# Performance work log

Measured on AMD Instinct MI355X. Metric: run time of the kernel, lower is better.

The kernel has to match this reference:

```python
import jax, jax.numpy as jnp
import numpy as np

B, S, E, H, D, P = 4, 2048, 1024, 16, 64, 64  # batch, seq, embed, heads, head_dim, position_dim
MASKED_BIAS = -10000.0


def setup_inputs() -> dict:
    key = jax.random.key(0)
    ks = jax.random.split(key, 24)
    n = lambda k, sh: jax.random.normal(k, sh, dtype=jnp.float32)
    eyeD = jnp.eye(D, dtype=jnp.float32)
    eyeH = jnp.eye(H, dtype=jnp.float32)
    inp = {
        'hidden_states': n(ks[0], (B, S, E)),
        'position_states': n(ks[1], (B, S, P)),
        # Conv2D per-head projections (identity init + perturbation): [H, D, D]
        'Wq': eyeD[None] + 0.02 * n(ks[2], (H, D, D)), 'bq': 0.01 * n(ks[3], (H, D)),
        'Wk': eyeD[None] + 0.02 * n(ks[4], (H, D, D)), 'bk': 0.01 * n(ks[5], (H, D)),
        'Wv': eyeD[None] + 0.02 * n(ks[6], (H, D, D)), 'bv': 0.01 * n(ks[7], (H, D)),
        # Conv2D(transpose=True) cross-head mix: weight [H_out, H_in, D], bias [H, D]
        'Wqh': eyeH[:, :, None] + 0.02 * n(ks[8], (H, H, D)), 'bqh': 0.01 * n(ks[9], (H, D)),
        'Wkh': eyeH[:, :, None] + 0.02 * n(ks[10], (H, H, D)), 'bkh': 0.01 * n(ks[11], (H, D)),
        'Wvh': eyeH[:, :, None] + 0.02 * n(ks[12], (H, H, D)), 'bvh': 0.01 * n(ks[13], (H, D)),
        # p_attn Conv1D: position_dim -> 3*head_dim
        'Wp': 0.02 * n(ks[14], (P, 3 * D)), 'bp': 0.01 * n(ks[15], (3 * D,)),
        # position_conv expand: weight [3, 1, H], bias [H]
        'Wpe': 0.02 * n(ks[16], (3, 1, H)), 'bpe': 0.01 * n(ks[17], (H,)),
        # c_proj Conv1D: E -> E
        'Wc': 0.02 * n(ks[18], (E, E)), 'bc': 0.01 * n(ks[19], (E,)),
    }
    return inp


def _attention(hidden_states, position_states, Wq, bq, Wqh, bqh, Wk, bk, Wkh, bkh,
               Wv, bv, Wvh, bvh, Wp, bp, Wpe, bpe, Wc, bc):
    b, s, _ = hidden_states.shape
    x = hidden_states.reshape(b, s, H, D)

    def proj(Wa, ba, Wh, bh):
        # Conv2D: per-head linear within head_dim
        y = jnp.einsum('bshd,hde->bshe', x, Wa) + ba
        # Conv2D(transpose): mix across heads, per feature dim d
        return jnp.einsum('bshd,ghd->bsgd', y, Wh) + bh

    q = proj(Wq, bq, Wqh, bqh)  # [b,s,H,D]
    k = proj(Wk, bk, Wkh, bkh)
    v = proj(Wv, bv, Wvh, bvh)

    # p_attn (Conv1D) -> [b,s,3,D]; p_expand broadcasts each var across heads
    p = (position_states @ Wp + bp).reshape(b, s, 3, D)
    pe = p[..., None, :] * Wpe[:, 0, :][:, :, None] + bpe[:, None]  # [b,s,3,H,D]
    q = q + pe[:, :, 0]
    k = k + pe[:, :, 1]
    v = v + pe[:, :, 2]

    q = q.transpose(0, 2, 1, 3)  # [b,H,s,D]
    k = k.transpose(0, 2, 1, 3)
    v = v.transpose(0, 2, 1, 3)

    scores = jnp.einsum('bhqd,bhkd->bhqk', q, k) / jnp.sqrt(jnp.float32(D))
    causal = jnp.tril(jnp.ones((s, s), dtype=bool))
    scores = jnp.where(causal, scores, jnp.float32(MASKED_BIAS))
    w = jax.nn.softmax(scores, axis=-1)
    o = jnp.einsum('bhqk,bhkd->bhqd', w, v)
    o = o.transpose(0, 2, 1, 3).reshape(b, s, E)
    return o @ Wc + bc


def reference(hidden_states, position_states, Wq, bq, Wqh, bqh, Wk, bk, Wkh, bkh,
              Wv, bv, Wvh, bvh, Wp, bp, Wpe, bpe, Wc, bc):
    return _attention(hidden_states, position_states, Wq, bq, Wqh, bqh, Wk, bk,
                      Wkh, bkh, Wv, bv, Wvh, bvh, Wp, bp, Wpe, bpe, Wc, bc)
```

## Files before the change

### kernel.cpp

```cpp
#include <hip/hip_runtime.h>
#include <stdint.h>
#include <stddef.h>

using bf16x8 = __attribute__((ext_vector_type(8))) __bf16;
using f32x4  = __attribute__((ext_vector_type(4))) float;
using u16x8  = __attribute__((ext_vector_type(8))) unsigned short;
using u16x4  = __attribute__((ext_vector_type(4))) unsigned short;
typedef unsigned short u16;

#define DEV __device__ __forceinline__

#define QSCALE 0.18033688011112042f
#define SBIAS 32.0f

DEV u16 f2bf(float f) {
  unsigned u = __float_as_uint(f);
  u += 0x7fffu + ((u >> 16) & 1u);
  return (u16)(u >> 16);
}

DEV void gld_lds16(const u16* g, u16* l) {
  __builtin_amdgcn_global_load_lds(
      (__attribute__((address_space(1))) void*)g,
      (__attribute__((address_space(3))) void*)l, 16, 0, 0);
}

__global__ __launch_bounds__(256) void k_prep(const float* __restrict__ hs, const float* __restrict__ ps,
                                              const float* __restrict__ Wq, const float* __restrict__ Wk,
                                              const float* __restrict__ Wv, const float* __restrict__ Wqh,
                                              const float* __restrict__ Wkh, const float* __restrict__ Wvh,
                                              const float* __restrict__ Wp, const float* __restrict__ Wpe,
                                              const float* __restrict__ bq, const float* __restrict__ bk,
                                              const float* __restrict__ bv, const float* __restrict__ bqh,
                                              const float* __restrict__ bkh, const float* __restrict__ bvh,
                                              const float* __restrict__ bp, const float* __restrict__ bpe,
                                              const float* __restrict__ Wc,
                                              u16* __restrict__ A, u16* __restrict__ Wt,
                                              float* __restrict__ bias, u16* __restrict__ WcT) {
  const int bid = blockIdx.x;
  if (bid < 8704) {
    int idx = bid * 256 + threadIdx.x;
    int t  = idx / 272;
    int c4 = (idx - t * 272) * 4;
    float4 f;
    if (c4 < 1024) f = *(const float4*)(hs + (size_t)t * 1024 + c4);
    else           f = *(const float4*)(ps + (size_t)t * 64 + (c4 - 1024));
    u16x4 o4;
    o4[0] = f2bf(f.x); o4[1] = f2bf(f.y); o4[2] = f2bf(f.z); o4[3] = f2bf(f.w);
    *(u16x4*)(A + (size_t)t * 1088 + c4) = o4;
  } else if (bid < 21760) {
    int idx = (bid - 8704) * 256 + threadIdx.x;
    int n = idx / 1088, kk = idx - n * 1088;
    int which = n >> 10, g = (n >> 6) & 15, e = n & 63;
    const float* Wa = (which == 0) ? Wq : (which == 1) ? Wk : Wv;
    const float* Wh = (which == 0) ? Wqh : (which == 1) ? Wkh : Wvh;
    float val;
    if (kk < 1024) {
      int h = kk >> 6, d = kk & 63;
      val = Wa[(size_t)(h * 64 + d) * 64 + e] * Wh[(size_t)(g * 16 + h) * 64 + e];
    } else {
      int p = kk - 1024;
      val = Wp[(size_t)p * 192 + which * 64 + e] * Wpe[which * 16 + g];
    }
    if (which == 0) val *= QSCALE;
    Wt[idx] = f2bf(val);
  } else if (bid < 21772) {
    int n = (bid - 21760) * 256 + threadIdx.x;
    int which = n >> 10, g = (n >> 6) & 15, e = n & 63;
    const float* ba = (which == 0) ? bq : (which == 1) ? bk : bv;
    const float* Wh = (which == 0) ? Wqh : (which == 1) ? Wkh : Wvh;
    const float* bh = (which == 0) ? bqh : (which == 1) ? bkh : bvh;
    float s = bh[g * 64 + e] + bp[which * 64 + e] * Wpe[which * 16 + g] + bpe[g];
    for (int h = 0; h < 16; ++h) s += ba[h * 64 + e] * Wh[(g * 16 + h) * 64 + e];
    if (which == 0) s *= QSCALE;
    bias[n] = s;
  } else {
    __shared__ float tile[32][33];
    int t = bid - 21772;
    int tx = threadIdx.x & 31, ty = threadIdx.x >> 5;
    int n0 = (t & 31) * 32, k0 = (t >> 5) * 32;
#pragma unroll
    for (int i = 0; i < 32; i += 8)
      tile[ty + i][tx] = Wc[(size_t)(k0 + ty + i) * 1024 + n0 + tx];
    __syncthreads();
#pragma unroll
    for (int i = 0; i < 32; i += 8)
      WcT[(size_t)(n0 + ty + i) * 1024 + k0 + tx] = f2bf(tile[tx][ty + i]);
  }
}

template <int EPI>
__global__ __launch_bounds__(256) void gemm128(const u16* __restrict__ A, const u16* __restrict__ Bt,
                                               const float* __restrict__ bias,
                                               u16* __restrict__ qo, u16* __restrict__ ko, u16* __restrict__ vo,
                                               float* __restrict__ outf, int M, int N, int K, int NT) {
  __shared__ alignas(16) u16 As[2][8192];
  __shared__ alignas(16) u16 Bs[2][8192];
  const int tid = threadIdx.x;
  const int l = tid & 63, w = tid >> 6;
  const int lr = l & 15, lg = l >> 4;
  const int wm = w >> 1, wn = w & 1;

  const int nwg = gridDim.x;
  const int cpx = nwg >> 3;
  const int virt = (blockIdx.x & 7) * cpx + (blockIdx.x >> 3);
  const int m0 = (virt / NT) * 128, n0 = (virt - (virt / NT) * NT) * 128;

  const int KT = K >> 6;

  f32x4 acc[4][4] = {};

#pragma unroll
  for (int call = 0; call < 4; ++call) {
    int ci = (call * 4 + w) * 64 + l;
    int row = ci >> 3, s = ci & 7;
    int kq = (s ^ (row & 7)) * 8;
    gld_lds16(A + (size_t)(m0 + row) * K + kq, &As[0][(call * 4 + w) * 512]);
    gld_lds16(Bt + (size_t)(n0 + row) * K + kq, &Bs[0][(call * 4 + w) * 512]);
  }

  int cur = 0;
  for (int kt = 0; kt < KT; ++kt) {
    if (kt + 1 < KT) {
      const int kb = (kt + 1) * 64;
#pragma unroll
      for (int call = 0; call < 4; ++call) {
        int ci = (call * 4 + w) * 64 + l;
        int row = ci >> 3, s = ci & 7;
        int kq = (s ^ (row & 7)) * 8;
        gld_lds16(A + (size_t)(m0 + row) * K + kb + kq, &As[cur ^ 1][(call * 4 + w) * 512]);
        gld_lds16(Bt + (size_t)(n0 + row) * K + kb + kq, &Bs[cur ^ 1][(call * 4 + w) * 512]);
      }
      asm volatile("s_waitcnt vmcnt(8)" ::: "memory");
    } else {
      asm volatile("s_waitcnt vmcnt(0)" ::: "memory");
    }
    __builtin_amdgcn_s_barrier();
    asm volatile("" ::: "memory");

    const u16* AsC = As[cur];
    const u16* BsC = Bs[cur];
#pragma unroll
    for (int kk = 0; kk < 2; ++kk) {
      bf16x8 af[4], bfr[4];
#pragma unroll
      for (int mf = 0; mf < 4; ++mf) {
        int row = wm * 64 + mf * 16 + lr;
        int byo = row * 128 + (((kk * 32 + lg * 8) * 2) ^ ((row & 7) << 4));
        af[mf] = *(const bf16x8*)((const char*)AsC + byo);
      }
#pragma unroll
      for (int nf = 0; nf < 4; ++nf) {
        int row = wn * 64 + nf * 16 + lr;
        int byo = row * 128 + (((kk * 32 + lg * 8) * 2) ^ ((row & 7) << 4));
        bfr[nf] = *(const bf16x8*)((const char*)BsC + byo);
      }
      __builtin_amdgcn_s_setprio(1);
#pragma unroll
      for (int mf = 0; mf < 4; ++mf)
#pragma unroll
        for (int nf = 0; nf < 4; ++nf)
          acc[mf][nf] = __builtin_amdgcn_mfma_f32_16x16x32_bf16(af[mf], bfr[nf], acc[mf][nf], 0, 0, 0);
      __builtin_amdgcn_s_setprio(0);
    }

    asm volatile("s_waitcnt lgkmcnt(0)" ::: "memory");
    __builtin_amdgcn_s_barrier();
    asm volatile("" ::: "memory");
    cur ^= 1;
  }

#pragma unroll
  for (int mf = 0; mf < 4; ++mf)
#pragma unroll
    for (int nf = 0; nf < 4; ++nf)
#pragma unroll
      for (int r = 0; r < 4; ++r) {
        int row = m0 + wm * 64 + mf * 16 + lg * 4 + r;
        int col = n0 + wn * 64 + nf * 16 + lr;
        float val = acc[mf][nf][r] + bias[col];
        if (EPI == 0) {
          int which = col >> 10, g = (col >> 6) & 15, e = col & 63;
          int b = row >> 11, si = row & 2047;
          size_t idx = ((size_t)((b * 16 + g) * 2048 + si)) * 64 + e;
          u16 bvv = f2bf(val);
          if (which == 0) qo[idx] = bvv;
          else if (which == 1) ko[idx] = bvv;
          else vo[idx] = bvv;
        } else {
          outf[(size_t)row * N + col] = val;
        }
      }
}

__global__ __launch_bounds__(256) void k_transV(const u16* __restrict__ v, u16* __restrict__ vT) {
  __shared__ u16 t[64][65];
  int bh = blockIdx.y, s0 = blockIdx.x * 64;
  const u16* src = v + ((size_t)bh * 2048 + s0) * 64;
  u16* dst = vT + (size_t)bh * 64 * 2048 + s0;
  int tid = threadIdx.x;
#pragma unroll
  for (int it = 0; it < 2; ++it) {
    int ci = it * 256 + tid;
    int row = ci >> 3, sl = ci & 7;
    u16x8 val = *(const u16x8*)(src + (size_t)row * 64 + sl * 8);
#pragma unroll
    for (int jj = 0; jj < 8; ++jj) t[row][sl * 8 + jj] = val[jj];
  }
  __syncthreads();
#pragma unroll
  for (int it = 0; it < 2; ++it) {
    int ci = it * 256 + tid;
    int d = ci >> 3, sl = ci & 7;
    u16x8 val;
#pragma unroll
    for (int jj = 0; jj < 8; ++jj) {
      int cp = sl * 8 + jj;
      int tt = (cp & 3) * 16 + (cp >> 2);
      val[jj] = t[tt][d];
    }
    *(u16x8*)(dst + (size_t)d * 2048 + sl * 8) = val;
  }
}

__global__ __launch_bounds__(512) void k_attn(const u16* __restrict__ q, const u16* __restrict__ k,
                                              const u16* __restrict__ vt, u16* __restrict__ o) {
  __shared__ alignas(16) u16 Ks[2][4096];
  __shared__ alignas(16) u16 Vs[2][4096];
  __shared__ alignas(16) u16 Ps[8][32 * 72];

  const int tid = threadIdx.x, l = tid & 63, w = tid >> 6;
  const int lr = l & 15, lg = l >> 4;
  const int i = blockIdx.x;
  const int bh = (i & 7) * 8 + ((i >> 3) & 7);
  const int xb = i >> 6;
  const int b = bh >> 4, h = bh & 15;

  const u16* qp = q + (size_t)bh * 2048 * 64;
  const u16* kp = k + (size_t)bh * 2048 * 64;
  const u16* vp = vt + (size_t)bh * 64 * 2048;

  const int srow = tid >> 3;
  const int skq = ((tid & 7) ^ (srow & 7)) * 8;

  bf16x8 ones;
#pragma unroll
  for (int e = 0; e < 8; ++e) ones[e] = (__bf16)1.0f;

  for (int half = 0; half < 2; ++half) {
    const int tile = half ? (7 - xb) : xb;
    const int qr0 = tile * 256 + w * 32;
    const int jmax = 4 * tile + 3;
    const int jmask = qr0 >> 6;

    bf16x8 qf[2][2];
#pragma unroll
    for (int mf = 0; mf < 2; ++mf)
#pragma unroll
      for (int kk = 0; kk < 2; ++kk)
        qf[mf][kk] = *(const bf16x8*)(qp + (size_t)(qr0 + mf * 16 + lr) * 64 + kk * 32 + lg * 8);

    f32x4 oacc[2][4] = {};
    f32x4 osum[2] = {};

    gld_lds16(kp + (size_t)srow * 64 + skq, &Ks[0][w * 512]);
    gld_lds16(vp + (size_t)srow * 2048 + skq, &Vs[0][w * 512]);

    int cur = 0;
    for (int j = 0; j <= jmax; ++j) {
      if (j < jmax) {
        const int jn = j + 1;
        gld_lds16(kp + (size_t)(jn * 64 + srow) * 64 + skq, &Ks[cur ^ 1][w * 512]);
        gld_lds16(vp + (size_t)srow * 2048 + jn * 64 + skq, &Vs[cur ^ 1][w * 512]);
        asm volatile("s_waitcnt vmcnt(2)" ::: "memory");
      } else {
        asm volatile("s_waitcnt vmcnt(0)" ::: "memory");
      }
      __builtin_amdgcn_s_barrier();
      asm volatile("" ::: "memory");

      if (j <= jmask) {
        const u16* KsC = Ks[cur];
        const u16* VsC = Vs[cur];

        f32x4 sfr[2][4];
#pragma unroll
        for (int mf = 0; mf < 2; ++mf)
#pragma unroll
          for (int nf = 0; nf < 4; ++nf)
            sfr[mf][nf] = f32x4{-SBIAS, -SBIAS, -SBIAS, -SBIAS};
#pragma unroll
        for (int kk = 0; kk < 2; ++kk) {
          bf16x8 bk[4];
#pragma unroll
          for (int nf = 0; nf < 4; ++nf) {
            int row = nf * 16 + lr;
            int byo = row * 128 + (((kk * 32 + lg * 8) * 2) ^ ((row & 7) << 4));
            bk[nf] = *(const bf16x8*)((const char*)KsC + byo);
          }
          __builtin_amdgcn_s_setprio(1);
#pragma unroll
          for (int mf = 0; mf < 2; ++mf)
#pragma unroll
            for (int nf = 0; nf < 4; ++nf)
              sfr[mf][nf] = __builtin_amdgcn_mfma_f32_16x16x32_bf16(qf[mf][kk], bk[nf], sfr[mf][nf], 0, 0, 0);
          __builtin_amdgcn_s_setprio(0);
        }

        const bool maskt = (j == jmask);
#pragma unroll
        for (int mf = 0; mf < 2; ++mf)
#pragma unroll
          for (int r = 0; r < 4; ++r) {
            float s0 = sfr[mf][0][r], s1 = sfr[mf][1][r], s2 = sfr[mf][2][r], s3 = sfr[mf][3][r];
            if (maskt) {
              int rowg = qr0 + mf * 16 + lg * 4 + r;
              int base = j * 64 + lr;
              if (base      > rowg) s0 = -1e30f;
              if (base + 16 > rowg) s1 = -1e30f;
              if (base + 32 > rowg) s2 = -1e30f;
              if (base + 48 > rowg) s3 = -1e30f;
            }
            float p0 = __builtin_amdgcn_exp2f(s0);
            float p1 = __builtin_amdgcn_exp2f(s1);
            float p2 = __builtin_amdgcn_exp2f(s2);
            float p3 = __builtin_amdgcn_exp2f(s3);
            unsigned w0, w1;
            asm("v_cvt_pk_bf16_f32 %0, %1, %2" : "=v"(w0) : "v"(p0), "v"(p1));
            asm("v_cvt_pk_bf16_f32 %0, %1, %2" : "=v"(w1) : "v"(p2), "v"(p3));
            uint2 pw; pw.x = w0; pw.y = w1;
            *(uint2*)&Ps[w][(mf * 16 + lg * 4 + r) * 72 + 4 * lr] = pw;
          }

#pragma unroll
        for (int kk = 0; kk < 2; ++kk) {
          bf16x8 pa[2];
#pragma unroll
          for (int mf = 0; mf < 2; ++mf)
            pa[mf] = *(const bf16x8*)&Ps[w][(mf * 16 + lr) * 72 + kk * 32 + lg * 8];
          bf16x8 bv[4];
#pragma unroll
          for (int df = 0; df < 4; ++df) {
            int row = df * 16 + lr;
            int byo = row * 128 + (((kk * 32 + lg * 8) * 2) ^ ((row & 7) << 4));
            bv[df] = *(const bf16x8*)((const char*)VsC + byo);
          }
          __builtin_amdgcn_s_setprio(1);
#pragma unroll
          for (int mf = 0; mf < 2; ++mf)
#pragma unroll
            for (int df = 0; df < 4; ++df)
              oacc[mf][df] = __builtin_amdgcn_mfma_f32_16x16x32_bf16(pa[mf], bv[df], oacc[mf][df], 0, 0, 0);
#pragma unroll
          for (int mf = 0; mf < 2; ++mf)
            osum[mf] = __builtin_amdgcn_mfma_f32_16x16x32_bf16(pa[mf], ones, osum[mf], 0, 0, 0);
          __builtin_amdgcn_s_setprio(0);
        }
      }

      asm volatile("s_waitcnt lgkmcnt(0)" ::: "memory");
      __builtin_amdgcn_s_barrier();
      asm volatile("" ::: "memory");
      cur ^= 1;
    }

#pragma unroll
    for (int mf = 0; mf < 2; ++mf)
#pragma unroll
      for (int r = 0; r < 4; ++r) {
        float inv = 1.0f / osum[mf][r];
        int rowg = qr0 + mf * 16 + lg * 4 + r;
#pragma unroll
        for (int df = 0; df < 4; ++df)
          o[((size_t)(b * 2048 + rowg)) * 1024 + h * 64 + df * 16 + lr] = f2bf(oacc[mf][df][r] * inv);
      }
  }
}

extern "C" void kernel_launch(void* const* d_in, const int* in_sizes, int n_in,
                              void* d_out, int out_size, void* d_ws, size_t ws_size,
                              hipStream_t stream) {
  const float* hs  = (const float*)d_in[0];
  const float* pos = (const float*)d_in[1];
  const float* Wq  = (const float*)d_in[2];  const float* bq  = (const float*)d_in[3];
  const float* Wk  = (const float*)d_in[4];  const float* bk  = (const float*)d_in[5];
  const float* Wv  = (const float*)d_in[6];  const float* bv  = (const float*)d_in[7];
  const float* Wqh = (const float*)d_in[8];  const float* bqh = (const float*)d_in[9];
  const float* Wkh = (const float*)d_in[10]; const float* bkh = (const float*)d_in[11];
  const float* Wvh = (const float*)d_in[12]; const float* bvh = (const float*)d_in[13];
  const float* Wp  = (const float*)d_in[14]; const float* bp  = (const float*)d_in[15];
  const float* Wpe = (const float*)d_in[16]; const float* bpe = (const float*)d_in[17];
  const float* Wc  = (const float*)d_in[18]; const float* bc  = (const float*)d_in[19];
  float* out = (float*)d_out;
  char* ws = (char*)d_ws;

  u16*   Abf   = (u16*)  (ws + 0);
  u16*   WT    = (u16*)  (ws + 17825792);
  float* biasq = (float*)(ws + 24510464);
  u16*   WcT   = (u16*)  (ws + 24522752);
  u16*   qb_   = (u16*)  (ws + 26619904);
  u16*   kb_   = (u16*)  (ws + 43397120);
  u16*   vb_   = (u16*)  (ws + 60174336);
  u16*   vTb   = (u16*)  (ws + 76951552);
  u16*   ob    = Abf;

  k_prep<<<22796, 256, 0, stream>>>(hs, pos, Wq, Wk, Wv, Wqh, Wkh, Wvh, Wp, Wpe,
                                    bq, bk, bv, bqh, bkh, bvh, bp, bpe, Wc,
                                    Abf, WT, biasq, WcT);
  gemm128<0><<<1536, 256, 0, stream>>>(Abf, WT, biasq, qb_, kb_, vb_, nullptr, 8192, 3072, 1088, 24);
  k_transV<<<dim3(32, 64), 256, 0, stream>>>(vb_, vTb);
  k_attn<<<256, 512, 0, stream>>>(qb_, kb_, vTb, ob);
  gemm128<1><<<512, 256, 0, stream>>>(ob, WcT, bc, nullptr, nullptr, nullptr, out, 8192, 1024, 1024, 8);
}
```

Before: 182.7 us.

## Add dedicated 256x192-tile QKV GEMM with B fragments loaded directly into registers

Replaces the templated 128x128 GEMM for the fused QKV projection with a new 512-thread kernel using 256x192 output tiles. Only A is staged through double-buffered swizzled LDS, while each wave streams its B fragments straight from global memory into registers with a one-step prefetch. The grid drops from 1536 to 512 workgroups. The aim is higher arithmetic intensity per workgroup and less LDS traffic and synchronisation. In exchange the kernel uses more registers per thread (8x3 accumulators plus 12 B vectors) and relies on hand-tuned vmcnt waits. The output-projection GEMM is de-templated to keep only the float epilogue.

```diff
diff --git a/kernel.cpp b/kernel.cpp
--- a/kernel.cpp
+++ b/kernel.cpp
@@ -89,10 +89,117 @@
   }
 }
 
-template <int EPI>
+__global__ __launch_bounds__(512) void gemmQKV(const u16* __restrict__ A, const u16* __restrict__ Bt,
+                                               const float* __restrict__ bias,
+                                               u16* __restrict__ qo, u16* __restrict__ ko, u16* __restrict__ vo,
+                                               int M, int N, int K, int NT) {
+  __shared__ alignas(16) u16 As[2][16384];
+  const int tid = threadIdx.x;
+  const int l = tid & 63, w = tid >> 6;
+  const int lr = l & 15, lg = l >> 4;
+  const int wm = w >> 2, wn = w & 3;
+
+  const int cpx = gridDim.x >> 3;
+  const int virt = (blockIdx.x & 7) * cpx + (blockIdx.x >> 3);
+  const int m0 = (virt / NT) * 256, n0 = (virt - (virt / NT) * NT) * 192;
+
+  const int KT = K >> 6;
+  const u16* bbase = Bt + (size_t)(n0 + wn * 48 + lr) * K + lg * 8;
+
+  f32x4 acc[8][3] = {};
+  bf16x8 bc0, bc1, bc2, bc3, bc4, bc5;
+  bf16x8 bn0, bn1, bn2, bn3, bn4, bn5;
+
+  bn0 = *(const bf16x8*)(bbase + (size_t)0 * K);
+  bn1 = *(const bf16x8*)(bbase + (size_t)0 * K + 32);
+  bn2 = *(const bf16x8*)(bbase + (size_t)16 * K);
+  bn3 = *(const bf16x8*)(bbase + (size_t)16 * K + 32);
+  bn4 = *(const bf16x8*)(bbase + (size_t)32 * K);
+  bn5 = *(const bf16x8*)(bbase + (size_t)32 * K + 32);
+#pragma unroll
+  for (int c = 0; c < 4; ++c) {
+    int ci = c * 512 + tid;
+    int row = ci >> 3, s = ci & 7;
+    int kq = (s ^ (row & 7)) * 8;
+    gld_lds16(A + (size_t)(m0 + row) * K + kq, &As[0][(c * 8 + w) * 512]);
+  }
+
+  for (int t = 0; t < KT; ++t) {
+    const int buf = t & 1;
+    asm volatile("s_waitcnt vmcnt(4)" ::: "memory");
+    bc0 = bn0; bc1 = bn1; bc2 = bn2; bc3 = bn3; bc4 = bn4; bc5 = bn5;
+    if (t + 1 < KT) {
+      const int kb = (t + 1) * 64;
+      bn0 = *(const bf16x8*)(bbase + (size_t)0 * K + kb);
+      bn1 = *(const bf16x8*)(bbase + (size_t)0 * K + kb + 32);
+      bn2 = *(const bf16x8*)(bbase + (size_t)16 * K + kb);
+      bn3 = *(const bf16x8*)(bbase + (size_t)16 * K + kb + 32);
+      bn4 = *(const bf16x8*)(bbase + (size_t)32 * K + kb);
+      bn5 = *(const bf16x8*)(bbase + (size_t)32 * K + kb + 32);
+#pragma unroll
+      for (int c = 0; c < 4; ++c) {
+        int ci = c * 512 + tid;
+        int row = ci >> 3, s = ci & 7;
+        int kq = (s ^ (row & 7)) * 8;
+        gld_lds16(A + (size_t)(m0 + row) * K + kb + kq, &As[buf ^ 1][(c * 8 + w) * 512]);
+      }
+      asm volatile("s_waitcnt vmcnt(10)" ::: "memory");
+    } else {
+      asm volatile("s_waitcnt vmcnt(0)" ::: "memory");
+    }
+    __builtin_amdgcn_s_barrier();
+    asm volatile("" ::: "memory");
+
+    const char* AsC = (const char*)As[buf];
+#pragma unroll
+    for (int kk = 0; kk < 2; ++kk) {
+      bf16x8 af[4];
+#pragma unroll
+      for (int half = 0; half < 2; ++half) {
+#pragma unroll
+        for (int mq = 0; mq < 4; ++mq) {
+          int row = wm * 128 + (half * 4 + mq) * 16 + lr;
+          int byo = row * 128 + (((kk * 32 + lg * 8) * 2) ^ ((row & 7) << 4));
+          af[mq] = *(const bf16x8*)(AsC + byo);
+        }
+        __builtin_amdgcn_s_setprio(1);
+#pragma unroll
+        for (int mq = 0; mq < 4; ++mq) {
+          int mf = half * 4 + mq;
+          acc[mf][0] = __builtin_amdgcn_mfma_f32_16x16x32_bf16(af[mq], kk ? bc1 : bc0, acc[mf][0], 0, 0, 0);
+          acc[mf][1] = __builtin_amdgcn_mfma_f32_16x16x32_bf16(af[mq], kk ? bc3 : bc2, acc[mf][1], 0, 0, 0);
+          acc[mf][2] = __builtin_amdgcn_mfma_f32_16x16x32_bf16(af[mq], kk ? bc5 : bc4, acc[mf][2], 0, 0, 0);
+        }
+        __builtin_amdgcn_s_setprio(0);
+      }
+    }
+
+    asm volatile("s_waitcnt lgkmcnt(0)" ::: "memory");
+    __builtin_amdgcn_s_barrier();
+    asm volatile("" ::: "memory");
+  }
+
+#pragma unroll
+  for (int mf = 0; mf < 8; ++mf)
+#pragma unroll
+    for (int nf = 0; nf < 3; ++nf)
+#pragma unroll
+      for (int r = 0; r < 4; ++r) {
+        int row = m0 + wm * 128 + mf * 16 + lg * 4 + r;
+        int col = n0 + wn * 48 + nf * 16 + lr;
+        float val = acc[mf][nf][r] + bias[col];
+        int which = col >> 10, g = (col >> 6) & 15, e = col & 63;
+        int b = row >> 11, si = row & 2047;
+        size_t idx = ((size_t)((b * 16 + g) * 2048 + si)) * 64 + e;
+        u16 bvv = f2bf(val);
+        if (which == 0) qo[idx] = bvv;
+        else if (which == 1) ko[idx] = bvv;
+        else vo[idx] = bvv;
+      }
+}
+
 __global__ __launch_bounds__(256) void gemm128(const u16* __restrict__ A, const u16* __restrict__ Bt,
                                                const float* __restrict__ bias,
-                                               u16* __restrict__ qo, u16* __restrict__ ko, u16* __restrict__ vo,
                                                float* __restrict__ outf, int M, int N, int K, int NT) {
   __shared__ alignas(16) u16 As[2][8192];
   __shared__ alignas(16) u16 Bs[2][8192];
@@ -178,18 +285,7 @@
       for (int r = 0; r < 4; ++r) {
         int row = m0 + wm * 64 + mf * 16 + lg * 4 + r;
         int col = n0 + wn * 64 + nf * 16 + lr;
-        float val = acc[mf][nf][r] + bias[col];
-        if (EPI == 0) {
-          int which = col >> 10, g = (col >> 6) & 15, e = col & 63;
-          int b = row >> 11, si = row & 2047;
-          size_t idx = ((size_t)((b * 16 + g) * 2048 + si)) * 64 + e;
-          u16 bvv = f2bf(val);
-          if (which == 0) qo[idx] = bvv;
-          else if (which == 1) ko[idx] = bvv;
-          else vo[idx] = bvv;
-        } else {
-          outf[(size_t)row * N + col] = val;
-        }
+        outf[(size_t)row * N + col] = acc[mf][nf][r] + bias[col];
       }
 }
 
@@ -407,8 +503,8 @@
   k_prep<<<22796, 256, 0, stream>>>(hs, pos, Wq, Wk, Wv, Wqh, Wkh, Wvh, Wp, Wpe,
                                     bq, bk, bv, bqh, bkh, bvh, bp, bpe, Wc,
                                     Abf, WT, biasq, WcT);
-  gemm128<0><<<1536, 256, 0, stream>>>(Abf, WT, biasq, qb_, kb_, vb_, nullptr, 8192, 3072, 1088, 24);
+  gemmQKV<<<512, 512, 0, stream>>>(Abf, WT, biasq, qb_, kb_, vb_, 8192, 3072, 1088, 16);
   k_transV<<<dim3(32, 64), 256, 0, stream>>>(vb_, vTb);
   k_attn<<<256, 512, 0, stream>>>(qb_, kb_, vTb, ob);
-  gemm128<1><<<512, 256, 0, stream>>>(ob, WcT, bc, nullptr, nullptr, nullptr, out, 8192, 1024, 1024, 8);
-}
+  gemm128<<<512, 256, 0, stream>>>(ob, WcT, bc, out, 8192, 1024, 1024, 8);
+}
```

Result: slower. 205.9 us (+12.7%).
